# Kernel tuning notes

Measured on AMD Instinct MI355X. Metric: run time of the kernel, lower is better.

Reference implementation:

```python
import jax, jax.numpy as jnp
import numpy as np

N, E = 50000, 800000
C_IN, C_HID, C_OUT = 64, 128, 64
BN_EPS = 1e-5


def setup_inputs() -> dict:
    key = jax.random.key(0)
    ks = jax.random.split(key, 8)
    s1 = 1.0 / np.sqrt(C_IN)
    s2 = 1.0 / np.sqrt(C_HID)
    return {
        "x": jax.random.normal(ks[0], (N, C_IN), dtype=jnp.float32),
        "edge_index": jax.random.randint(ks[1], (2, E), 0, N, dtype=jnp.int64),
        # message MLP: in -> hidden -> out
        "W1": jax.random.uniform(ks[2], (C_IN, C_HID), jnp.float32, -s1, s1),
        "b1": jnp.zeros((C_HID,), jnp.float32),
        "W2": jax.random.uniform(ks[3], (C_HID, C_OUT), jnp.float32, -s2, s2),
        "b2": jnp.zeros((C_OUT,), jnp.float32),
        # root/self transform
        "W_root": jax.random.uniform(ks[4], (C_IN, C_OUT), jnp.float32, -s1, s1),
        "b_root": jnp.zeros((C_OUT,), jnp.float32),
        # PReLU (single shared parameter, torch default 0.25)
        "prelu_w": jnp.full((1,), 0.25, jnp.float32),
        # BatchNorm affine params
        "bn_gamma": jnp.ones((C_OUT,), jnp.float32),
        "bn_beta": jnp.zeros((C_OUT,), jnp.float32),
    }


def reference(x, edge_index, W1, b1, W2, b2, W_root, b_root, prelu_w, bn_gamma, bn_beta):
    src, dst = edge_index[0], edge_index[1]
    # gather -> per-edge message MLP: [E, C_hid] -> [E, C_out]
    m = jax.nn.relu(x[src] @ W1 + b1) @ W2 + b2
    # scatter-sum to destination nodes: [N, C_out]
    agg = jax.ops.segment_sum(m, dst, num_segments=N)
    h = agg + x @ W_root + b_root
    # PReLU
    h = jnp.where(h >= 0, h, prelu_w * h)
    # BatchNorm over nodes (training-mode batch stats, biased var)
    mu = jnp.mean(h, axis=0)
    var = jnp.mean(jnp.square(h - mu), axis=0)
    h = (h - mu) * jax.lax.rsqrt(var + BN_EPS) * bn_gamma + bn_beta
    return h
```

## Files before the change

### kernel.cpp

```cpp
#include <hip/hip_runtime.h>

#define NNODES 50000
#define NEDGES 800000
#define NTILES 3125
#define CAP    64

typedef __attribute__((ext_vector_type(8))) short bf16x8;
typedef __attribute__((ext_vector_type(4))) float f32x4;

union FragU { uint u[4]; bf16x8 v; };

__device__ __forceinline__ uint bfr(float f) {
    uint u = __float_as_uint(f);
    return (u + 0x7fffu + ((u >> 16) & 1u)) >> 16;
}
__device__ __forceinline__ uint pack_bf2(float a, float b) {
    return bfr(a) | (bfr(b) << 16);
}
__device__ __forceinline__ float bf2f(uint hi16) {
    return __uint_as_float(hi16 << 16);
}

__global__ __launch_bounds__(256) void prep_kernel(
    const float* __restrict__ W1, const float* __restrict__ b1,
    const float* __restrict__ W2, const float* __restrict__ b2,
    const float* __restrict__ Wr, const float* __restrict__ br,
    uint* __restrict__ tbl, int* __restrict__ cnt, float* __restrict__ stats)
{
    const int f = blockIdx.x;
    const int tid = threadIdx.x;
    if (f < 40) {
        const int ln = tid >> 2, dd = tid & 3;
        const int g = ln >> 4, r = ln & 15;
        const int j0 = 2 * dd;
        float w0, w1v;
        if (f < 16) {
            const int mt = f >> 1, ks = f & 1;
            const int k = 32 * ks + 8 * g + j0, c = 16 * mt + r;
            w0 = W1[k * 128 + c];  w1v = W1[(k + 1) * 128 + c];
        } else if (f < 32) {
            const int mt = (f - 16) >> 2, ks = (f - 16) & 3;
            const int k = 32 * ks + 8 * g + j0, c = 16 * mt + r;
            w0 = W2[k * 64 + c];   w1v = W2[(k + 1) * 64 + c];
        } else {
            const int mt = (f - 32) >> 1, ks = (f - 32) & 1;
            const int k = 32 * ks + 8 * g + j0, c = 16 * mt + r;
            w0 = Wr[k * 64 + c];   w1v = Wr[(k + 1) * 64 + c];
        }
        tbl[f * 256 + tid] = pack_bf2(w0, w1v);
    } else if (f == 40) {
        if (tid < 128) tbl[10240 + tid] = __float_as_uint(b1[tid]);
        if (tid < 64) {
            tbl[10368 + tid] = __float_as_uint(b2[tid]);
            tbl[10432 + tid] = __float_as_uint(br[tid]);
        }
    } else {
        const int idx = (f - 41) * 256 + tid;
        if (idx < NNODES) cnt[idx] = 0;
        if (f == 41 && tid < 128) stats[tid] = 0.f;
    }
}

__global__ __launch_bounds__(256) void mlp_root_kernel(
    const float* __restrict__ x, const uint* __restrict__ tbl,
    ushort* __restrict__ M16, float* __restrict__ R)
{
    __shared__ uint  sH[4 * 16 * 68];
    __shared__ float sb[256];

    const int tid = threadIdx.x;
    if (tid < 128) {
        sb[tid]       = __uint_as_float(tbl[10240 + tid]);
        sb[128 + tid] = __uint_as_float(tbl[10368 + tid]);
    }
    __syncthreads();
    const float* sb1 = sb;
    const float* sb2 = sb + 128;
    const float* sbr = sb + 192;

    const int lane = tid & 63;
    const int g = lane >> 4, r = lane & 15;
    uint* Hw = &sH[(tid >> 6) * 16 * 68];
    uint* Mu = (uint*)M16;

#define LDTBL(f) (*(const bf16x8*)&tbl[((f) << 8) | (lane << 2)])

    bf16x8 wf[32];
#pragma unroll
    for (int f = 0; f < 32; ++f) wf[f] = LDTBL(f);

    const int gw  = blockIdx.x * 4 + (tid >> 6);
    const int nwv = gridDim.x * 4;

    for (int t = gw; t < NTILES; t += nwv) {
        const int node = t * 16 + r;
        bf16x8 xf[2];
#pragma unroll
        for (int ks = 0; ks < 2; ++ks) {
            const float4 f0 = *(const float4*)&x[node * 64 + 32 * ks + 8 * g];
            const float4 f1 = *(const float4*)&x[node * 64 + 32 * ks + 8 * g + 4];
            FragU fx;
            fx.u[0] = pack_bf2(f0.x, f0.y); fx.u[1] = pack_bf2(f0.z, f0.w);
            fx.u[2] = pack_bf2(f1.x, f1.y); fx.u[3] = pack_bf2(f1.z, f1.w);
            xf[ks] = fx.v;
        }
#pragma unroll
        for (int mt = 0; mt < 8; ++mt) {
            f32x4 a = {0.f, 0.f, 0.f, 0.f};
            a = __builtin_amdgcn_mfma_f32_16x16x32_bf16(wf[2 * mt], xf[0], a, 0, 0, 0);
            a = __builtin_amdgcn_mfma_f32_16x16x32_bf16(wf[2 * mt + 1], xf[1], a, 0, 0, 0);
            const int hc = 16 * mt + 4 * g;
            const float v0 = fmaxf(a[0] + sb1[hc + 0], 0.f);
            const float v1 = fmaxf(a[1] + sb1[hc + 1], 0.f);
            const float v2 = fmaxf(a[2] + sb1[hc + 2], 0.f);
            const float v3 = fmaxf(a[3] + sb1[hc + 3], 0.f);
            const int hd = r * 68 + 8 * mt + 2 * g;
            Hw[hd]     = pack_bf2(v0, v1);
            Hw[hd + 1] = pack_bf2(v2, v3);
        }
        bf16x8 hf[4];
#pragma unroll
        for (int ks = 0; ks < 4; ++ks)
            hf[ks] = *(const bf16x8*)&Hw[r * 68 + 16 * ks + 4 * g];
#pragma unroll
        for (int mt = 0; mt < 4; ++mt) {
            f32x4 a2 = {0.f, 0.f, 0.f, 0.f};
#pragma unroll
            for (int ks = 0; ks < 4; ++ks)
                a2 = __builtin_amdgcn_mfma_f32_16x16x32_bf16(wf[16 + 4 * mt + ks], hf[ks], a2, 0, 0, 0);
            f32x4 ar = {0.f, 0.f, 0.f, 0.f};
            ar = __builtin_amdgcn_mfma_f32_16x16x32_bf16(LDTBL(32 + 2 * mt), xf[0], ar, 0, 0, 0);
            ar = __builtin_amdgcn_mfma_f32_16x16x32_bf16(LDTBL(32 + 2 * mt + 1), xf[1], ar, 0, 0, 0);
            const int oc = 16 * mt + 4 * g;
            const float m0 = a2[0] + sb2[oc + 0], m1 = a2[1] + sb2[oc + 1];
            const float m2 = a2[2] + sb2[oc + 2], m3 = a2[3] + sb2[oc + 3];
            uint2 mp = make_uint2(pack_bf2(m0, m1), pack_bf2(m2, m3));
            *(uint2*)&Mu[node * 32 + 8 * mt + 2 * g] = mp;
            float4 rv = make_float4(ar[0] + sbr[oc + 0], ar[1] + sbr[oc + 1],
                                    ar[2] + sbr[oc + 2], ar[3] + sbr[oc + 3]);
            *(float4*)&R[node * 64 + oc] = rv;
        }
    }
#undef LDTBL
}

__global__ __launch_bounds__(256) void fill_kernel(
    const int* __restrict__ ei, int* __restrict__ cnt, ushort* __restrict__ bucketU)
{
    const int e = blockIdx.x * 256 + threadIdx.x;
    const int dst = ei[NEDGES + e];
    const int pos = atomicAdd(&cnt[dst], 1);
    if (pos < CAP) bucketU[dst * CAP + pos] = (ushort)ei[e];
}

__device__ __forceinline__ void burst_load(const uint2* __restrict__ M8, int sv,
                                           int c, int q, int u, uint2 mv[8])
{
#pragma unroll
    for (int j = 0; j < 4; ++j) {
        const int idx = 4 * j + q;
        const int s = __shfl(sv, (idx < c) ? idx : 0);
        mv[j] = M8[s * 16 + u];
    }
    if (c > 16) {
#pragma unroll
        for (int j = 4; j < 8; ++j) {
            const int idx = 4 * j + q;
            const int s = __shfl(sv, (idx < c) ? idx : 0);
            mv[j] = M8[s * 16 + u];
        }
    }
}

__device__ __forceinline__ void unpack_acc(const uint2 mv[8], int c, int q, int u,
                                           const uint2* __restrict__ M8, int sv,
                                           float& A0, float& A1, float& A2, float& A3)
{
    float a0 = 0.f, a1 = 0.f, a2 = 0.f, a3 = 0.f;
    float b0 = 0.f, b1 = 0.f, b2 = 0.f, b3 = 0.f;
#pragma unroll
    for (int j = 0; j < 4; ++j) {
        const bool ok = (4 * j + q) < c;
        const uint lo = ok ? mv[j].x : 0u;
        const uint hi = ok ? mv[j].y : 0u;
        if (j & 1) { b0 += bf2f(lo & 0xffffu); b1 += bf2f(lo >> 16);
                     b2 += bf2f(hi & 0xffffu); b3 += bf2f(hi >> 16); }
        else       { a0 += bf2f(lo & 0xffffu); a1 += bf2f(lo >> 16);
                     a2 += bf2f(hi & 0xffffu); a3 += bf2f(hi >> 16); }
    }
    if (c > 16) {
#pragma unroll
        for (int j = 4; j < 8; ++j) {
            const bool ok = (4 * j + q) < c;
            const uint lo = ok ? mv[j].x : 0u;
            const uint hi = ok ? mv[j].y : 0u;
            if (j & 1) { b0 += bf2f(lo & 0xffffu); b1 += bf2f(lo >> 16);
                         b2 += bf2f(hi & 0xffffu); b3 += bf2f(hi >> 16); }
            else       { a0 += bf2f(lo & 0xffffu); a1 += bf2f(lo >> 16);
                         a2 += bf2f(hi & 0xffffu); a3 += bf2f(hi >> 16); }
        }
        if (c > 32) {
            for (int i = 32; i < c; i += 4) {
                const int idx = i + q;
                const int s = __shfl(sv, (idx < c) ? idx : 0);
                const uint2 m = M8[s * 16 + u];
                const bool ok = idx < c;
                const uint lo = ok ? m.x : 0u;
                const uint hi = ok ? m.y : 0u;
                a0 += bf2f(lo & 0xffffu); a1 += bf2f(lo >> 16);
                a2 += bf2f(hi & 0xffffu); a3 += bf2f(hi >> 16);
            }
        }
    }
    A0 = a0 + b0; A1 = a1 + b1; A2 = a2 + b2; A3 = a3 + b3;
}

__device__ __forceinline__ void combine_store(float a0, float a1, float a2, float a3,
                                              float hv, float p, int lane,
                                              float* __restrict__ hrow,
                                              float& sum, float& sumsq)
{
    a0 += __shfl_xor(a0, 16); a0 += __shfl_xor(a0, 32);
    a1 += __shfl_xor(a1, 16); a1 += __shfl_xor(a1, 32);
    a2 += __shfl_xor(a2, 16); a2 += __shfl_xor(a2, 32);
    a3 += __shfl_xor(a3, 16); a3 += __shfl_xor(a3, 32);
    const int srcl = lane >> 2;
    const float t0 = __shfl(a0, srcl), t1 = __shfl(a1, srcl);
    const float t2 = __shfl(a2, srcl), t3 = __shfl(a3, srcl);
    const float e01 = (lane & 1) ? t1 : t0;
    const float e23 = (lane & 1) ? t3 : t2;
    float v = hv + ((lane & 2) ? e23 : e01);
    v = (v >= 0.f) ? v : p * v;
    hrow[lane] = v;
    sum += v;
    sumsq = fmaf(v, v, sumsq);
}

__global__ __launch_bounds__(256) void gather_prelu_stats_kernel(
    const int* __restrict__ cnt, const ushort* __restrict__ bucketU,
    const uint2* __restrict__ M8, const float* __restrict__ pw,
    float* __restrict__ h, float* __restrict__ stats)
{
    __shared__ float ls[128];
    const int tid = threadIdx.x;
    if (tid < 128) ls[tid] = 0.f;
    __syncthreads();

    const int lane = tid & 63;
    const int q    = lane >> 4;
    const int u    = lane & 15;
    const int gw   = (blockIdx.x * 256 + tid) >> 6;
    const int nwv  = (gridDim.x * 256) >> 6;
    const float p  = pw[0];
    float sum = 0.f, sumsq = 0.f;

    int nA = gw, nB = gw + nwv;
    int cA = 0, svA = 0; float hA = 0.f;
    if (nA < NNODES) { cA = cnt[nA]; svA = (int)bucketU[nA * 64 + lane]; hA = h[nA * 64 + lane]; }
    int cB = 0, svB = 0; float hB = 0.f;
    if (nB < NNODES) { cB = cnt[nB]; svB = (int)bucketU[nB * 64 + lane]; hB = h[nB * 64 + lane]; }

    while (nA < NNODES) {
        const int  ca   = cA > CAP ? CAP : cA;
        const int  cb   = cB > CAP ? CAP : cB;
        const bool hasB = nB < NNODES;

        uint2 mvA[8], mvB[8];
        burst_load(M8, svA, ca, q, u, mvA);
        if (hasB) burst_load(M8, svB, cb, q, u, mvB);

        const int n2 = nA + 2 * nwv, n3 = nB + 2 * nwv;
        int c2 = 0, s2 = 0; float h2 = 0.f;
        int c3 = 0, s3 = 0; float h3 = 0.f;
        if (n2 < NNODES) { c2 = cnt[n2]; s2 = (int)bucketU[n2 * 64 + lane]; h2 = h[n2 * 64 + lane]; }
        if (n3 < NNODES) { c3 = cnt[n3]; s3 = (int)bucketU[n3 * 64 + lane]; h3 = h[n3 * 64 + lane]; }

        float A0, A1, A2, A3;
        unpack_acc(mvA, ca, q, u, M8, svA, A0, A1, A2, A3);
        combine_store(A0, A1, A2, A3, hA, p, lane, &h[nA * 64], sum, sumsq);

        if (hasB) {
            float B0, B1, B2, B3;
            unpack_acc(mvB, cb, q, u, M8, svB, B0, B1, B2, B3);
            combine_store(B0, B1, B2, B3, hB, p, lane, &h[nB * 64], sum, sumsq);
        }

        nA = n2; nB = n3;
        cA = c2; svA = s2; hA = h2;
        cB = c3; svB = s3; hB = h3;
    }
    atomicAdd(&ls[lane], sum);
    atomicAdd(&ls[64 + lane], sumsq);
    __syncthreads();
    if (tid < 128) atomicAdd(&stats[tid], ls[tid]);
}

__global__ __launch_bounds__(256) void bn_kernel(
    float4* __restrict__ h, const float* __restrict__ stats,
    const float* __restrict__ gamma, const float* __restrict__ beta)
{
    const int i  = blockIdx.x * 256 + threadIdx.x;
    const int c0 = (i & 15) * 4;
    const float inv = 1.0f / (float)NNODES;
    const float4 s1 = *(const float4*)&stats[c0];
    const float4 s2 = *(const float4*)&stats[64 + c0];
    const float4 gm = *(const float4*)&gamma[c0];
    const float4 bt = *(const float4*)&beta[c0];
    float4 v = h[i];
    float mu, var;
    mu = s1.x * inv; var = s2.x * inv - mu * mu; v.x = (v.x - mu) * (gm.x * rsqrtf(var + 1e-5f)) + bt.x;
    mu = s1.y * inv; var = s2.y * inv - mu * mu; v.y = (v.y - mu) * (gm.y * rsqrtf(var + 1e-5f)) + bt.y;
    mu = s1.z * inv; var = s2.z * inv - mu * mu; v.z = (v.z - mu) * (gm.z * rsqrtf(var + 1e-5f)) + bt.z;
    mu = s1.w * inv; var = s2.w * inv - mu * mu; v.w = (v.w - mu) * (gm.w * rsqrtf(var + 1e-5f)) + bt.w;
    h[i] = v;
}

extern "C" void kernel_launch(void* const* d_in, const int* in_sizes, int n_in,
                              void* d_out, int out_size, void* d_ws, size_t ws_size,
                              hipStream_t stream) {
    const float* x     = (const float*)d_in[0];
    const int*   ei    = (const int*)d_in[1];
    const float* W1    = (const float*)d_in[2];
    const float* b1    = (const float*)d_in[3];
    const float* W2    = (const float*)d_in[4];
    const float* b2    = (const float*)d_in[5];
    const float* Wr    = (const float*)d_in[6];
    const float* br    = (const float*)d_in[7];
    const float* pw    = (const float*)d_in[8];
    const float* gamma = (const float*)d_in[9];
    const float* beta  = (const float*)d_in[10];

    float* out = (float*)d_out;

    char* ws = (char*)d_ws;
    ushort* M16    = (ushort*)ws;
    ushort* bucketU= (ushort*)(ws + 6400000);
    int*    cnt    = (int*)(ws + 12800000);
    float*  stats  = (float*)(ws + 12800000 + 200000);
    uint*   tbl    = (uint*)(ws + 12800000 + 200000 + 512);

    prep_kernel<<<237, 256, 0, stream>>>(W1, b1, W2, b2, Wr, br, tbl, cnt, stats);
    fill_kernel<<<NEDGES / 256, 256, 0, stream>>>(ei, cnt, bucketU);
    mlp_root_kernel<<<256, 256, 0, stream>>>(x, tbl, M16, out);
    gather_prelu_stats_kernel<<<2048, 256, 0, stream>>>(cnt, bucketU, (const uint2*)M16, pw, out, stats);
    bn_kernel<<<3125, 256, 0, stream>>>((float4*)out, stats, gamma, beta);
}
```

Measured before the change: 203.1 us.

## Split bf16 messages into channel halves and gather each half in separate passes

The MLP kernel now writes per-node bf16 messages as two separate 32-channel arrays, each 3.2 MB. The gather kernel is launched twice, once per half. Each wave handles two nodes and loads 4-byte chunks instead of 8-byte ones. The aim is for each pass's random-gather working set to fit better in L2/LLC so fewer gathers miss the cache. The cost is reading the bucket and count arrays twice and paying an extra kernel launch.

After: 213.8 us. 5.2% more time.

```diff
diff --git a/kernel.cpp b/kernel.cpp
--- a/kernel.cpp
+++ b/kernel.cpp
@@ -63,7 +63,7 @@
 
 __global__ __launch_bounds__(256) void mlp_root_kernel(
     const float* __restrict__ x, const uint* __restrict__ tbl,
-    ushort* __restrict__ M16, float* __restrict__ R)
+    uint* __restrict__ MuL, uint* __restrict__ MuH, float* __restrict__ R)
 {
     __shared__ uint  sH[4 * 16 * 68];
     __shared__ float sb[256];
@@ -81,7 +81,6 @@
     const int lane = tid & 63;
     const int g = lane >> 4, r = lane & 15;
     uint* Hw = &sH[(tid >> 6) * 16 * 68];
-    uint* Mu = (uint*)M16;
 
 #define LDTBL(f) (*(const bf16x8*)&tbl[((f) << 8) | (lane << 2)])
 
@@ -135,7 +134,8 @@
             const float m0 = a2[0] + sb2[oc + 0], m1 = a2[1] + sb2[oc + 1];
             const float m2 = a2[2] + sb2[oc + 2], m3 = a2[3] + sb2[oc + 3];
             uint2 mp = make_uint2(pack_bf2(m0, m1), pack_bf2(m2, m3));
-            *(uint2*)&Mu[node * 32 + 8 * mt + 2 * g] = mp;
+            uint* dst = (mt < 2) ? MuL : MuH;
+            *(uint2*)&dst[node * 16 + 8 * (mt & 1) + 2 * g] = mp;
             float4 rv = make_float4(ar[0] + sbr[oc + 0], ar[1] + sbr[oc + 1],
                                     ar[2] + sbr[oc + 2], ar[3] + sbr[oc + 3]);
             *(float4*)&R[node * 64 + oc] = rv;
@@ -153,146 +153,155 @@
     if (pos < CAP) bucketU[dst * CAP + pos] = (ushort)ei[e];
 }
 
-__device__ __forceinline__ void burst_load(const uint2* __restrict__ M8, int sv,
-                                           int c, int q, int u, uint2 mv[8])
-{
-#pragma unroll
-    for (int j = 0; j < 4; ++j) {
-        const int idx = 4 * j + q;
-        const int s = __shfl(sv, (idx < c) ? idx : 0);
-        mv[j] = M8[s * 16 + u];
-    }
-    if (c > 16) {
-#pragma unroll
-        for (int j = 4; j < 8; ++j) {
-            const int idx = 4 * j + q;
-            const int s = __shfl(sv, (idx < c) ? idx : 0);
-            mv[j] = M8[s * 16 + u];
-        }
-    }
-}
-
-__device__ __forceinline__ void unpack_acc(const uint2 mv[8], int c, int q, int u,
-                                           const uint2* __restrict__ M8, int sv,
-                                           float& A0, float& A1, float& A2, float& A3)
-{
-    float a0 = 0.f, a1 = 0.f, a2 = 0.f, a3 = 0.f;
-    float b0 = 0.f, b1 = 0.f, b2 = 0.f, b3 = 0.f;
-#pragma unroll
-    for (int j = 0; j < 4; ++j) {
-        const bool ok = (4 * j + q) < c;
-        const uint lo = ok ? mv[j].x : 0u;
-        const uint hi = ok ? mv[j].y : 0u;
-        if (j & 1) { b0 += bf2f(lo & 0xffffu); b1 += bf2f(lo >> 16);
-                     b2 += bf2f(hi & 0xffffu); b3 += bf2f(hi >> 16); }
-        else       { a0 += bf2f(lo & 0xffffu); a1 += bf2f(lo >> 16);
-                     a2 += bf2f(hi & 0xffffu); a3 += bf2f(hi >> 16); }
-    }
-    if (c > 16) {
-#pragma unroll
-        for (int j = 4; j < 8; ++j) {
-            const bool ok = (4 * j + q) < c;
-            const uint lo = ok ? mv[j].x : 0u;
-            const uint hi = ok ? mv[j].y : 0u;
-            if (j & 1) { b0 += bf2f(lo & 0xffffu); b1 += bf2f(lo >> 16);
-                         b2 += bf2f(hi & 0xffffu); b3 += bf2f(hi >> 16); }
-            else       { a0 += bf2f(lo & 0xffffu); a1 += bf2f(lo >> 16);
-                         a2 += bf2f(hi & 0xffffu); a3 += bf2f(hi >> 16); }
-        }
-        if (c > 32) {
-            for (int i = 32; i < c; i += 4) {
-                const int idx = i + q;
-                const int s = __shfl(sv, (idx < c) ? idx : 0);
-                const uint2 m = M8[s * 16 + u];
-                const bool ok = idx < c;
-                const uint lo = ok ? m.x : 0u;
-                const uint hi = ok ? m.y : 0u;
-                a0 += bf2f(lo & 0xffffu); a1 += bf2f(lo >> 16);
-                a2 += bf2f(hi & 0xffffu); a3 += bf2f(hi >> 16);
-            }
-        }
-    }
-    A0 = a0 + b0; A1 = a1 + b1; A2 = a2 + b2; A3 = a3 + b3;
-}
-
-__device__ __forceinline__ void combine_store(float a0, float a1, float a2, float a3,
-                                              float hv, float p, int lane,
-                                              float* __restrict__ hrow,
-                                              float& sum, float& sumsq)
-{
-    a0 += __shfl_xor(a0, 16); a0 += __shfl_xor(a0, 32);
-    a1 += __shfl_xor(a1, 16); a1 += __shfl_xor(a1, 32);
-    a2 += __shfl_xor(a2, 16); a2 += __shfl_xor(a2, 32);
-    a3 += __shfl_xor(a3, 16); a3 += __shfl_xor(a3, 32);
-    const int srcl = lane >> 2;
-    const float t0 = __shfl(a0, srcl), t1 = __shfl(a1, srcl);
-    const float t2 = __shfl(a2, srcl), t3 = __shfl(a3, srcl);
-    const float e01 = (lane & 1) ? t1 : t0;
-    const float e23 = (lane & 1) ? t3 : t2;
-    float v = hv + ((lane & 2) ? e23 : e01);
-    v = (v >= 0.f) ? v : p * v;
-    hrow[lane] = v;
-    sum += v;
-    sumsq = fmaf(v, v, sumsq);
-}
-
-__global__ __launch_bounds__(256) void gather_prelu_stats_kernel(
+__global__ __launch_bounds__(256) void gather_half_kernel(
     const int* __restrict__ cnt, const ushort* __restrict__ bucketU,
-    const uint2* __restrict__ M8, const float* __restrict__ pw,
-    float* __restrict__ h, float* __restrict__ stats)
-{
-    __shared__ float ls[128];
+    const uint* __restrict__ Mh, const float* __restrict__ pw,
+    float* __restrict__ h, float* __restrict__ stats, const int choff)
+{
+    __shared__ float ls[64];
     const int tid = threadIdx.x;
-    if (tid < 128) ls[tid] = 0.f;
+    if (tid < 64) ls[tid] = 0.f;
     __syncthreads();
 
     const int lane = tid & 63;
     const int q    = lane >> 4;
     const int u    = lane & 15;
+    const int isB  = lane >> 5;
+    const int ch   = lane & 31;
+    const float p  = pw[0];
     const int gw   = (blockIdx.x * 256 + tid) >> 6;
     const int nwv  = (gridDim.x * 256) >> 6;
-    const float p  = pw[0];
     float sum = 0.f, sumsq = 0.f;
 
-    int nA = gw, nB = gw + nwv;
-    int cA = 0, svA = 0; float hA = 0.f;
-    if (nA < NNODES) { cA = cnt[nA]; svA = (int)bucketU[nA * 64 + lane]; hA = h[nA * 64 + lane]; }
-    int cB = 0, svB = 0; float hB = 0.f;
-    if (nB < NNODES) { cB = cnt[nB]; svB = (int)bucketU[nB * 64 + lane]; hB = h[nB * 64 + lane]; }
-
-    while (nA < NNODES) {
-        const int  ca   = cA > CAP ? CAP : cA;
-        const int  cb   = cB > CAP ? CAP : cB;
-        const bool hasB = nB < NNODES;
-
-        uint2 mvA[8], mvB[8];
-        burst_load(M8, svA, ca, q, u, mvA);
-        if (hasB) burst_load(M8, svB, cb, q, u, mvB);
-
-        const int n2 = nA + 2 * nwv, n3 = nB + 2 * nwv;
-        int c2 = 0, s2 = 0; float h2 = 0.f;
-        int c3 = 0, s3 = 0; float h3 = 0.f;
-        if (n2 < NNODES) { c2 = cnt[n2]; s2 = (int)bucketU[n2 * 64 + lane]; h2 = h[n2 * 64 + lane]; }
-        if (n3 < NNODES) { c3 = cnt[n3]; s3 = (int)bucketU[n3 * 64 + lane]; h3 = h[n3 * 64 + lane]; }
-
-        float A0, A1, A2, A3;
-        unpack_acc(mvA, ca, q, u, M8, svA, A0, A1, A2, A3);
-        combine_store(A0, A1, A2, A3, hA, p, lane, &h[nA * 64], sum, sumsq);
-
-        if (hasB) {
-            float B0, B1, B2, B3;
-            unpack_acc(mvB, cb, q, u, M8, svB, B0, B1, B2, B3);
-            combine_store(B0, B1, B2, B3, hB, p, lane, &h[nB * 64], sum, sumsq);
-        }
-
-        nA = n2; nB = n3;
-        cA = c2; svA = s2; hA = h2;
-        cB = c3; svB = s3; hB = h3;
-    }
-    atomicAdd(&ls[lane], sum);
-    atomicAdd(&ls[64 + lane], sumsq);
+    int pi = gw;
+    int cA = 0, svA = 0, cB = 0, svB = 0; float hv = 0.f;
+    if (2 * pi < NNODES) {
+        const int nA = 2 * pi;
+        cA = cnt[nA]; cB = cnt[nA + 1];
+        svA = (int)bucketU[nA * 64 + lane];
+        svB = (int)bucketU[(nA + 1) * 64 + lane];
+        hv  = h[(nA + isB) * 64 + choff + ch];
+    }
+
+    while (2 * pi < NNODES) {
+        const int nA = 2 * pi;
+        const int ca = cA > CAP ? CAP : cA;
+        const int cb = cB > CAP ? CAP : cB;
+
+        uint mvA[8], mvB[8];
+#pragma unroll
+        for (int j = 0; j < 4; ++j) {
+            const int ia = 4 * j + q;
+            mvA[j] = Mh[(uint)__shfl(svA, ia < ca ? ia : 0) * 16u + u];
+        }
+        if (ca > 16) {
+#pragma unroll
+            for (int j = 4; j < 8; ++j) {
+                const int ia = 4 * j + q;
+                mvA[j] = Mh[(uint)__shfl(svA, ia < ca ? ia : 0) * 16u + u];
+            }
+        }
+#pragma unroll
+        for (int j = 0; j < 4; ++j) {
+            const int ib = 4 * j + q;
+            mvB[j] = Mh[(uint)__shfl(svB, ib < cb ? ib : 0) * 16u + u];
+        }
+        if (cb > 16) {
+#pragma unroll
+            for (int j = 4; j < 8; ++j) {
+                const int ib = 4 * j + q;
+                mvB[j] = Mh[(uint)__shfl(svB, ib < cb ? ib : 0) * 16u + u];
+            }
+        }
+
+        const int pin = pi + nwv;
+        int c2 = 0, s2 = 0, c3 = 0, s3 = 0; float h2 = 0.f;
+        if (2 * pin < NNODES) {
+            const int n2 = 2 * pin;
+            c2 = cnt[n2]; c3 = cnt[n2 + 1];
+            s2 = (int)bucketU[n2 * 64 + lane];
+            s3 = (int)bucketU[(n2 + 1) * 64 + lane];
+            h2 = h[(n2 + isB) * 64 + choff + ch];
+        }
+
+        float a0A, a1A;
+        {
+            float a0 = 0.f, a1 = 0.f, x0 = 0.f, x1 = 0.f;
+#pragma unroll
+            for (int j = 0; j < 4; ++j) {
+                const uint v = ((4 * j + q) < ca) ? mvA[j] : 0u;
+                if (j & 1) { x0 += bf2f(v & 0xffffu); x1 += bf2f(v >> 16); }
+                else       { a0 += bf2f(v & 0xffffu); a1 += bf2f(v >> 16); }
+            }
+            if (ca > 16) {
+#pragma unroll
+                for (int j = 4; j < 8; ++j) {
+                    const uint v = ((4 * j + q) < ca) ? mvA[j] : 0u;
+                    if (j & 1) { x0 += bf2f(v & 0xffffu); x1 += bf2f(v >> 16); }
+                    else       { a0 += bf2f(v & 0xffffu); a1 += bf2f(v >> 16); }
+                }
+                if (ca > 32) {
+                    for (int i = 32; i < ca; i += 4) {
+                        const int idx = i + q;
+                        const uint mv = Mh[(uint)__shfl(svA, idx < ca ? idx : 0) * 16u + u];
+                        const uint v = (idx < ca) ? mv : 0u;
+                        a0 += bf2f(v & 0xffffu); a1 += bf2f(v >> 16);
+                    }
+                }
+            }
+            a0A = a0 + x0; a1A = a1 + x1;
+        }
+        float a0B, a1B;
+        {
+            float a0 = 0.f, a1 = 0.f, x0 = 0.f, x1 = 0.f;
+#pragma unroll
+            for (int j = 0; j < 4; ++j) {
+                const uint v = ((4 * j + q) < cb) ? mvB[j] : 0u;
+                if (j & 1) { x0 += bf2f(v & 0xffffu); x1 += bf2f(v >> 16); }
+                else       { a0 += bf2f(v & 0xffffu); a1 += bf2f(v >> 16); }
+            }
+            if (cb > 16) {
+#pragma unroll
+                for (int j = 4; j < 8; ++j) {
+                    const uint v = ((4 * j + q) < cb) ? mvB[j] : 0u;
+                    if (j & 1) { x0 += bf2f(v & 0xffffu); x1 += bf2f(v >> 16); }
+                    else       { a0 += bf2f(v & 0xffffu); a1 += bf2f(v >> 16); }
+                }
+                if (cb > 32) {
+                    for (int i = 32; i < cb; i += 4) {
+                        const int idx = i + q;
+                        const uint mv = Mh[(uint)__shfl(svB, idx < cb ? idx : 0) * 16u + u];
+                        const uint v = (idx < cb) ? mv : 0u;
+                        a0 += bf2f(v & 0xffffu); a1 += bf2f(v >> 16);
+                    }
+                }
+            }
+            a0B = a0 + x0; a1B = a1 + x1;
+        }
+
+        a0A += __shfl_xor(a0A, 16); a0A += __shfl_xor(a0A, 32);
+        a1A += __shfl_xor(a1A, 16); a1A += __shfl_xor(a1A, 32);
+        a0B += __shfl_xor(a0B, 16); a0B += __shfl_xor(a0B, 32);
+        a1B += __shfl_xor(a1B, 16); a1B += __shfl_xor(a1B, 32);
+
+        const int srcl = (ch >> 1) + (isB << 5);
+        const float sel0 = isB ? a0B : a0A;
+        const float sel1 = isB ? a1B : a1A;
+        const float t0 = __shfl(sel0, srcl);
+        const float t1 = __shfl(sel1, srcl);
+        float v = hv + ((ch & 1) ? t1 : t0);
+        v = (v >= 0.f) ? v : p * v;
+        h[(nA + isB) * 64 + choff + ch] = v;
+        sum += v;
+        sumsq = fmaf(v, v, sumsq);
+
+        pi = pin; cA = c2; svA = s2; cB = c3; svB = s3; hv = h2;
+    }
+    atomicAdd(&ls[ch], sum);
+    atomicAdd(&ls[32 + ch], sumsq);
     __syncthreads();
-    if (tid < 128) atomicAdd(&stats[tid], ls[tid]);
+    if (tid < 32)       atomicAdd(&stats[choff + tid], ls[tid]);
+    else if (tid < 64)  atomicAdd(&stats[64 + choff + (tid - 32)], ls[tid]);
 }
 
 __global__ __launch_bounds__(256) void bn_kernel(
@@ -333,15 +342,17 @@
     float* out = (float*)d_out;
 
     char* ws = (char*)d_ws;
-    ushort* M16    = (ushort*)ws;
+    uint*   M_lo   = (uint*)ws;
+    uint*   M_hi   = (uint*)(ws + 3200000);
     ushort* bucketU= (ushort*)(ws + 6400000);
     int*    cnt    = (int*)(ws + 12800000);
-    float*  stats  = (float*)(ws + 12800000 + 200000);
-    uint*   tbl    = (uint*)(ws + 12800000 + 200000 + 512);
+    float*  stats  = (float*)(ws + 13000000);
+    uint*   tbl    = (uint*)(ws + 13000512);
 
     prep_kernel<<<237, 256, 0, stream>>>(W1, b1, W2, b2, Wr, br, tbl, cnt, stats);
     fill_kernel<<<NEDGES / 256, 256, 0, stream>>>(ei, cnt, bucketU);
-    mlp_root_kernel<<<256, 256, 0, stream>>>(x, tbl, M16, out);
-    gather_prelu_stats_kernel<<<2048, 256, 0, stream>>>(cnt, bucketU, (const uint2*)M16, pw, out, stats);
+    mlp_root_kernel<<<256, 256, 0, stream>>>(x, tbl, M_lo, M_hi, out);
+    gather_half_kernel<<<2048, 256, 0, stream>>>(cnt, bucketU, M_lo, pw, out, stats, 0);
+    gather_half_kernel<<<2048, 256, 0, stream>>>(cnt, bucketU, M_hi, pw, out, stats, 32);
     bn_kernel<<<3125, 256, 0, stream>>>((float4*)out, stats, gamma, beta);
 }
```

## Fuse edge bucket fill and MLP/root transform into one heterogeneous launch

Applied to the files above, without the earlier changes.

Merges the edge-bucketing fill kernel and the per-node MLP/root MFMA kernel into a single launch. The first 625 blocks do the atomic bucket fill, with each thread handling 5 edges. The remaining 256 blocks do the MLP tiles. This removes a kernel launch boundary and lets the atomic-bound fill run alongside the compute-bound MFMA work. The fill blocks share the kernel's register and LDS footprint, which could limit occupancy for the fill portion.

Result: slower. 207.8 us (+2.3%).

```diff
diff --git a/kernel.cpp b/kernel.cpp
--- a/kernel.cpp
+++ b/kernel.cpp
@@ -4,6 +4,8 @@
 #define NEDGES 800000
 #define NTILES 3125
 #define CAP    64
+#define NFILLB 625
+#define NMLPB  256
 
 typedef __attribute__((ext_vector_type(8))) short bf16x8;
 typedef __attribute__((ext_vector_type(4))) float f32x4;
@@ -61,7 +63,8 @@
     }
 }
 
-__global__ __launch_bounds__(256) void mlp_root_kernel(
+__global__ __launch_bounds__(256) void fused_fill_mlp_kernel(
+    const int* __restrict__ ei, int* __restrict__ cnt, ushort* __restrict__ bucketU,
     const float* __restrict__ x, const uint* __restrict__ tbl,
     ushort* __restrict__ M16, float* __restrict__ R)
 {
@@ -69,6 +72,24 @@
     __shared__ float sb[256];
 
     const int tid = threadIdx.x;
+
+    if (blockIdx.x < NFILLB) {
+        const int t0 = blockIdx.x * 256 + tid;
+        int dst[5], src[5];
+#pragma unroll
+        for (int j = 0; j < 5; ++j) {
+            dst[j] = ei[NEDGES + t0 + j * 160000];
+            src[j] = ei[t0 + j * 160000];
+        }
+        int pos[5];
+#pragma unroll
+        for (int j = 0; j < 5; ++j) pos[j] = atomicAdd(&cnt[dst[j]], 1);
+#pragma unroll
+        for (int j = 0; j < 5; ++j)
+            if (pos[j] < CAP) bucketU[dst[j] * CAP + pos[j]] = (ushort)src[j];
+        return;
+    }
+
     if (tid < 128) {
         sb[tid]       = __uint_as_float(tbl[10240 + tid]);
         sb[128 + tid] = __uint_as_float(tbl[10368 + tid]);
@@ -89,8 +110,8 @@
 #pragma unroll
     for (int f = 0; f < 32; ++f) wf[f] = LDTBL(f);
 
-    const int gw  = blockIdx.x * 4 + (tid >> 6);
-    const int nwv = gridDim.x * 4;
+    const int gw  = (blockIdx.x - NFILLB) * 4 + (tid >> 6);
+    const int nwv = NMLPB * 4;
 
     for (int t = gw; t < NTILES; t += nwv) {
         const int node = t * 16 + r;
@@ -142,15 +163,6 @@
         }
     }
 #undef LDTBL
-}
-
-__global__ __launch_bounds__(256) void fill_kernel(
-    const int* __restrict__ ei, int* __restrict__ cnt, ushort* __restrict__ bucketU)
-{
-    const int e = blockIdx.x * 256 + threadIdx.x;
-    const int dst = ei[NEDGES + e];
-    const int pos = atomicAdd(&cnt[dst], 1);
-    if (pos < CAP) bucketU[dst * CAP + pos] = (ushort)ei[e];
 }
 
 __device__ __forceinline__ void burst_load(const uint2* __restrict__ M8, int sv,
@@ -336,12 +348,11 @@
     ushort* M16    = (ushort*)ws;
     ushort* bucketU= (ushort*)(ws + 6400000);
     int*    cnt    = (int*)(ws + 12800000);
-    float*  stats  = (float*)(ws + 12800000 + 200000);
-    uint*   tbl    = (uint*)(ws + 12800000 + 200000 + 512);
+    float*  stats  = (float*)(ws + 13000000);
+    uint*   tbl    = (uint*)(ws + 13000512);
 
     prep_kernel<<<237, 256, 0, stream>>>(W1, b1, W2, b2, Wr, br, tbl, cnt, stats);
-    fill_kernel<<<NEDGES / 256, 256, 0, stream>>>(ei, cnt, bucketU);
-    mlp_root_kernel<<<256, 256, 0, stream>>>(x, tbl, M16, out);
+    fused_fill_mlp_kernel<<<NFILLB + NMLPB, 256, 0, stream>>>(ei, cnt, bucketU, x, tbl, M16, out);
     gather_prelu_stats_kernel<<<2048, 256, 0, stream>>>(cnt, bucketU, (const uint2*)M16, pw, out, stats);
     bn_kernel<<<3125, 256, 0, stream>>>((float4*)out, stats, gamma, beta);
 }
```
